# Performance work log

Measured on AMD Instinct MI355X. Metric: run time of the kernel, lower is better.

## Reference

```python
import jax, jax.numpy as jnp
from jax import lax
import numpy as np

VOCAB, TAGS, EMB, HID = 50000, 45, 256, 512
B, S = 32, 256


def setup_inputs() -> dict:
    key = jax.random.key(0)
    ks = jax.random.split(key, 12)
    sc = 0.05
    return {
        "x": jax.random.randint(ks[0], (B, S), 0, VOCAB),
        "tags": jax.random.randint(ks[1], (B, S), 0, TAGS),
        "emb": jax.random.normal(ks[2], (VOCAB, EMB), jnp.float32) * sc,
        "w_ih_f": jax.random.normal(ks[3], (4 * HID, EMB), jnp.float32) * sc,
        "w_hh_f": jax.random.normal(ks[4], (4 * HID, HID), jnp.float32) * sc,
        "b_f": jnp.zeros((4 * HID,), jnp.float32),
        "w_ih_b": jax.random.normal(ks[5], (4 * HID, EMB), jnp.float32) * sc,
        "w_hh_b": jax.random.normal(ks[6], (4 * HID, HID), jnp.float32) * sc,
        "b_b": jnp.zeros((4 * HID,), jnp.float32),
        "lin_w": jax.random.normal(ks[7], (TAGS, 2 * HID), jnp.float32) * sc,
        "lin_b": jnp.zeros((TAGS,), jnp.float32),
        "start_t": jax.random.normal(ks[8], (TAGS,), jnp.float32) * 0.1,
        "end_t": jax.random.normal(ks[9], (TAGS,), jnp.float32) * 0.1,
        "trans": jax.random.normal(ks[10], (TAGS,), jnp.float32)[:, None] * 0.0 + jax.random.normal(ks[11], (TAGS, TAGS), jnp.float32) * 0.1,
    }


def _lstm_dir(xs, w_ih, w_hh, b, reverse):
    # xs: [B,S,E]. PyTorch gate order: i, f, g, o.
    Bsz = xs.shape[0]
    H = w_hh.shape[1]
    def step(carry, x_t):
        h, c = carry
        g = x_t @ w_ih.T + h @ w_hh.T + b
        i, f, gg, o = jnp.split(g, 4, axis=-1)
        c = jax.nn.sigmoid(f) * c + jax.nn.sigmoid(i) * jnp.tanh(gg)
        h = jax.nn.sigmoid(o) * jnp.tanh(c)
        return (h, c), h
    init = (jnp.zeros((Bsz, H), xs.dtype), jnp.zeros((Bsz, H), xs.dtype))
    _, hs = lax.scan(step, init, jnp.swapaxes(xs, 0, 1), reverse=reverse)
    return jnp.swapaxes(hs, 0, 1)  # [B,S,H]


def _crf_nll(em, tags, start_t, end_t, trans):
    # em: [B,S,T]; numerator: score of gold path
    em_sc = jnp.take_along_axis(em, tags[..., None], axis=2)[..., 0].sum(axis=1)
    tr_sc = trans[tags[:, :-1], tags[:, 1:]].sum(axis=1)
    score = start_t[tags[:, 0]] + em_sc + tr_sc + end_t[tags[:, -1]]
    # partition function via forward algorithm (logsumexp recurrence)
    alpha0 = start_t + em[:, 0]  # [B,T]
    def step(alpha, e_t):
        alpha = jax.nn.logsumexp(alpha[:, :, None] + trans[None], axis=1) + e_t
        return alpha, None
    alpha, _ = lax.scan(step, alpha0, jnp.swapaxes(em[:, 1:], 0, 1))
    logZ = jax.nn.logsumexp(alpha + end_t, axis=1)
    return -(score - logZ).mean()  # reduction='mean', loss = -llh


def reference(x, tags, emb, w_ih_f, w_hh_f, b_f, w_ih_b, w_hh_b, b_b,
              lin_w, lin_b, start_t, end_t, trans):
    embeds = emb[x]                               # [B,S,E]
    h_f = _lstm_dir(embeds, w_ih_f, w_hh_f, b_f, False)
    h_b = _lstm_dir(embeds, w_ih_b, w_hh_b, b_b, True)
    lstm_out = jnp.concatenate([h_f, h_b], axis=-1)  # [B,S,2H]
    emissions = lstm_out @ lin_w.T + lin_b           # [B,S,T]
    return _crf_nll(emissions, tags, start_t, end_t, trans)
```

## Files before the change

### kernel.cpp

```cpp
#include <hip/hip_runtime.h>

#define BB 32
#define SS 256
#define EMBD 256
#define HIDD 512
#define NTAG 45
#define TPAD 48
#define NBLK 32
#define ROWS 64
#define APAD 520
#define GRID_REC 256

typedef __bf16 bf16x8 __attribute__((ext_vector_type(8)));
typedef float  f32x4  __attribute__((ext_vector_type(4)));
typedef short  s16x8  __attribute__((ext_vector_type(8)));

__device__ __forceinline__ unsigned short f2bf(float x) {
  unsigned u = __builtin_bit_cast(unsigned, x);
  u = (u + 0x7fffu + ((u >> 16) & 1u)) >> 16;
  return (unsigned short)u;
}
__device__ __forceinline__ float bf2f(unsigned short u) {
  unsigned v = ((unsigned)u) << 16; return __builtin_bit_cast(float, v);
}

__device__ __forceinline__ unsigned ld32_cpol(const unsigned* p, bool sys) {
  unsigned v;
  if (sys) asm volatile("global_load_dword %0, %1, off sc0 sc1\ns_waitcnt vmcnt(0)"
                        : "=v"(v) : "v"(p) : "memory");
  else     asm volatile("global_load_dword %0, %1, off sc0\ns_waitcnt vmcnt(0)"
                        : "=v"(v) : "v"(p) : "memory");
  return v;
}
__device__ __forceinline__ void st32_cpol(unsigned* p, unsigned v, bool sys) {
  if (sys) asm volatile("global_store_dword %0, %1, off sc0 sc1" :: "v"(p), "v"(v) : "memory");
  else     asm volatile("global_store_dword %0, %1, off sc0"     :: "v"(p), "v"(v) : "memory");
}

#define LD8(CPOL)                                                           \
  asm volatile("global_load_dwordx4 %0, %[q0], off " CPOL "\n\t"            \
               "global_load_dwordx4 %1, %[q1], off " CPOL "\n\t"            \
               "global_load_dwordx4 %2, %[q2], off " CPOL "\n\t"            \
               "global_load_dwordx4 %3, %[q3], off " CPOL "\n\t"            \
               "global_load_dwordx4 %4, %[q4], off " CPOL "\n\t"            \
               "global_load_dwordx4 %5, %[q5], off " CPOL "\n\t"            \
               "global_load_dwordx4 %6, %[q6], off " CPOL "\n\t"            \
               "global_load_dwordx4 %7, %[q7], off " CPOL "\n\t"            \
               "s_waitcnt vmcnt(0)"                                         \
               : "=&v"(v0), "=&v"(v1), "=&v"(v2), "=&v"(v3),                \
                 "=&v"(v4), "=&v"(v5), "=&v"(v6), "=&v"(v7)                 \
               : [q0] "v"(p), [q1] "v"(p + 2048), [q2] "v"(p + 4096),       \
                 [q3] "v"(p + 6144), [q4] "v"(p + 8192), [q5] "v"(p + 10240),\
                 [q6] "v"(p + 12288), [q7] "v"(p + 14336)                   \
               : "memory")

__global__ void k_pack_e(const int* __restrict__ x, const float* __restrict__ emb,
                         unsigned short* __restrict__ E) {
  int idx = blockIdx.x * 256 + threadIdx.x;
  int e = idx & 255; int bt = idx >> 8; int b = bt & 31; int t = bt >> 5;
  int tok = x[b * SS + t];
  E[idx] = f2bf(emb[(long)tok * EMBD + e]);
}

__global__ void k_pack_w(const float* __restrict__ wih_f, const float* __restrict__ whh_f,
                         const float* __restrict__ bf_,  const float* __restrict__ wih_b,
                         const float* __restrict__ whh_b, const float* __restrict__ bb_,
                         unsigned short* __restrict__ Wh, unsigned short* __restrict__ Wie,
                         float* __restrict__ Bh) {
  long idx = (long)blockIdx.x * 256 + threadIdx.x;
  int k = (int)(idx % 768); long rest = idx / 768;
  int r2 = (int)(rest & 2047); int dir = (int)(rest >> 11);
  int blk = r2 >> 6, rl = r2 & 63, gate = rl >> 4, hl = rl & 15;
  int orig = gate * HIDD + blk * 16 + hl;
  const float* wih = dir ? wih_b : wih_f;
  const float* whh = dir ? whh_b : whh_f;
  if (k < HIDD) Wh[((long)(dir * 2048 + r2)) * 512 + k] = f2bf(whh[(long)orig * HIDD + k]);
  else          Wie[((long)(dir * 2048 + r2)) * 256 + (k - 512)] = f2bf(wih[(long)orig * EMBD + (k - 512)]);
  if (k == 0) {
    const float* bias = dir ? bb_ : bf_;
    Bh[dir * 2048 + r2] = bias[orig];
  }
}

__global__ void k_pack_l(const float* __restrict__ lin_w, const float* __restrict__ lin_b,
                         unsigned short* __restrict__ LW, float* __restrict__ LB) {
  int idx = blockIdx.x * 256 + threadIdx.x;
  if (idx < TPAD * 1024) {
    int tag = idx >> 10; int c = idx & 1023;
    LW[idx] = (tag < NTAG) ? f2bf(lin_w[tag * 1024 + c]) : (unsigned short)0;
  } else if (idx < TPAD * 1024 + TPAD) {
    int tag = idx - TPAD * 1024;
    LB[tag] = (tag < NTAG) ? lin_b[tag] : 0.f;
  }
}

__launch_bounds__(256)
__global__ void k_eproj(const unsigned short* __restrict__ E,
                        const unsigned short* __restrict__ Wie,
                        const float* __restrict__ Bh,
                        unsigned short* __restrict__ Ep) {
  __shared__ unsigned short W2[64 * 264];
  const int bx = blockIdx.x;
  const int tg = bx & 63, blk = (bx >> 6) & 31, dir = bx >> 11;
  const int tid = threadIdx.x;
  const int w = tid >> 6, lane = tid & 63;
  const int lm = lane & 15, quad = lane >> 4;

  {
    const unsigned short* src = Wie + ((long)(dir * 2048 + blk * 64)) * 256;
    for (int i = 0; i < 8; ++i) {
      int c = i * 256 + tid;
      int row = c >> 5, off = c & 31;
      *(s16x8*)&W2[row * 264 + off * 8] = *(const s16x8*)&src[row * 256 + off * 8];
    }
  }
  __syncthreads();

  f32x4 acc[2][4] = {};
#pragma unroll
  for (int kk = 0; kk < 8; ++kk) {
    s16x8 av[2];
#pragma unroll
    for (int sub = 0; sub < 2; ++sub)
      av[sub] = *(const s16x8*)&E[((long)(tg * 128 + w * 32 + sub * 16 + lm)) * 256 + kk * 32 + quad * 8];
#pragma unroll
    for (int sub = 0; sub < 2; ++sub)
#pragma unroll
      for (int n = 0; n < 4; ++n) {
        s16x8 bs = *(const s16x8*)&W2[(n * 16 + lm) * 264 + kk * 32 + quad * 8];
        acc[sub][n] = __builtin_amdgcn_mfma_f32_16x16x32_bf16(
            __builtin_bit_cast(bf16x8, av[sub]), __builtin_bit_cast(bf16x8, bs), acc[sub][n], 0, 0, 0);
      }
  }
  float bh[4];
#pragma unroll
  for (int n = 0; n < 4; ++n) bh[n] = Bh[dir * 2048 + blk * 64 + n * 16 + lm];
#pragma unroll
  for (int sub = 0; sub < 2; ++sub)
#pragma unroll
    for (int n = 0; n < 4; ++n)
#pragma unroll
      for (int r = 0; r < 4; ++r) {
        int m = w * 32 + sub * 16 + quad * 4 + r;
        int t = tg * 4 + (m >> 5), b = m & 31;
        int row_l = n * 16 + lm;
        Ep[((((long)(dir * 32 + blk) * 256 + t) * 32 + b) * 64) + row_l] =
            f2bf(acc[sub][n][r] + bh[n]);
      }
}

__launch_bounds__(256, 1)
__global__ void k_rec(const unsigned short* __restrict__ Wh,
                      const unsigned short* __restrict__ Ep,
                      unsigned short* __restrict__ H,
                      unsigned int* __restrict__ sync) {
  __shared__ unsigned short A_ls[32 * APAD];
  __shared__ float G_ls[32 * 66 + 4608];
  __shared__ int fast_ls;

  const int bx = blockIdx.x;
  const int role = bx & 7;
  if (role >= 2) return;
  const int dir = role;
  const int blk = bx >> 3;
  const int tid = threadIdx.x;
  const int w = tid >> 6, lane = tid & 63;
  const int lm = lane & 15, quad = lane >> 4;
  const int mt = w >> 1, nt = w & 1;

  unsigned int* det   = sync;
  unsigned int* flags = sync + 64;

  s16x8 wb[2][16];
  {
    const unsigned short* wsrc =
        Wh + ((long)(dir * 2048 + blk * 64 + nt * 32 + lm)) * 512 + quad * 8;
#pragma unroll
    for (int ns = 0; ns < 2; ++ns)
#pragma unroll
      for (int kk = 0; kk < 16; ++kk)
        wb[ns][kk] = *(const s16x8*)&wsrc[ns * 16 * 512 + kk * 32];
  }

  unsigned xcc;
  asm volatile("s_getreg_b32 %0, hwreg(HW_REG_XCC_ID)" : "=s"(xcc));
  if (tid == 0) st32_cpol(&det[dir * 32 + blk], xcc | 0x100u, true);
  if (w == 0) {
    unsigned v;
    for (;;) {
      v = (lane < 32) ? ld32_cpol(&det[dir * 32 + lane], true) : (xcc | 0x100u);
      if (__ballot(v != 0u) == ~0ull) break;
      __builtin_amdgcn_s_sleep(1);
    }
    if (lane == 0) fast_ls = (__ballot(v == (xcc | 0x100u)) == ~0ull) ? 1 : 0;
  }
  __syncthreads();
  const bool fast = (fast_ls != 0);
  __threadfence();

  const int gb = tid >> 3, hp = tid & 7;
  float c0 = 0.f, c1 = 0.f;

  unsigned short* Hd = H + (long)dir * SS * BB * HIDD;
  unsigned int* flagd = flags + dir * SS * NBLK;
  const unsigned short* Epd = Ep + ((long)(dir * 32 + blk) * 256) * 32 * 64;

  for (int t = 0; t < SS; ++t) {
    const int tE = (dir == 0) ? t : (SS - 1 - t);

    unsigned short epv[8];
    {
      const unsigned short* eb =
          Epd + ((long)tE * 32 + (mt * 16 + quad * 4)) * 64 + nt * 32 + lm;
#pragma unroll
      for (int ns = 0; ns < 2; ++ns)
#pragma unroll
        for (int r = 0; r < 4; ++r) epv[ns * 4 + r] = eb[r * 64 + ns * 16];
    }

    f32x4 acc0 = {0.f, 0.f, 0.f, 0.f}, acc1 = {0.f, 0.f, 0.f, 0.f};
    if (t > 0) {
      if (w == 0) {
        const unsigned int* fl = flagd + (long)(t - 1) * NBLK;
        for (;;) {
          unsigned f = (lane < 32) ? ld32_cpol(&fl[lane], !fast) : 1u;
          if (__ballot(f != 0u) == ~0ull) break;
          __builtin_amdgcn_s_sleep(1);
        }
      }
      __syncthreads();
      {
        const int hslot = (dir == 0) ? (t - 1) : (SS - t);
        const unsigned short* p = Hd + (long)hslot * BB * HIDD + w * 512 + lane * 8;
        s16x8 v0, v1, v2, v3, v4, v5, v6, v7;
        if (fast) { LD8("sc0"); } else { LD8("sc0 sc1"); }
        unsigned short* d = &A_ls[w * APAD + lane * 8];
        *(s16x8*)(d + 0 * 2080) = v0; *(s16x8*)(d + 1 * 2080) = v1;
        *(s16x8*)(d + 2 * 2080) = v2; *(s16x8*)(d + 3 * 2080) = v3;
        *(s16x8*)(d + 4 * 2080) = v4; *(s16x8*)(d + 5 * 2080) = v5;
        *(s16x8*)(d + 6 * 2080) = v6; *(s16x8*)(d + 7 * 2080) = v7;
      }
      __syncthreads();
#pragma unroll
      for (int kk = 0; kk < 16; ++kk) {
        s16x8 av = *(const s16x8*)&A_ls[(mt * 16 + lm) * APAD + kk * 32 + quad * 8];
        acc0 = __builtin_amdgcn_mfma_f32_16x16x32_bf16(
            __builtin_bit_cast(bf16x8, av), __builtin_bit_cast(bf16x8, wb[0][kk]), acc0, 0, 0, 0);
        acc1 = __builtin_amdgcn_mfma_f32_16x16x32_bf16(
            __builtin_bit_cast(bf16x8, av), __builtin_bit_cast(bf16x8, wb[1][kk]), acc1, 0, 0, 0);
      }
    }
#pragma unroll
    for (int r = 0; r < 4; ++r) {
      int mm = mt * 16 + quad * 4 + r;
      G_ls[mm * 66 + nt * 32 + lm]      = acc0[r] + bf2f(epv[r]);
      G_ls[mm * 66 + nt * 32 + 16 + lm] = acc1[r] + bf2f(epv[4 + r]);
    }
    __syncthreads();
    {
      float gi0 = G_ls[gb * 66 + 0  + 2 * hp], gi1 = G_ls[gb * 66 + 0  + 2 * hp + 1];
      float gf0 = G_ls[gb * 66 + 16 + 2 * hp], gf1 = G_ls[gb * 66 + 16 + 2 * hp + 1];
      float gg0 = G_ls[gb * 66 + 32 + 2 * hp], gg1 = G_ls[gb * 66 + 32 + 2 * hp + 1];
      float go0 = G_ls[gb * 66 + 48 + 2 * hp], go1 = G_ls[gb * 66 + 48 + 2 * hp + 1];
      float si0 = 1.f / (1.f + __expf(-gi0)), si1 = 1.f / (1.f + __expf(-gi1));
      float sf0 = 1.f / (1.f + __expf(-gf0)), sf1 = 1.f / (1.f + __expf(-gf1));
      float so0 = 1.f / (1.f + __expf(-go0)), so1 = 1.f / (1.f + __expf(-go1));
      float tg0 = tanhf(gg0), tg1 = tanhf(gg1);
      c0 = sf0 * c0 + si0 * tg0;
      c1 = sf1 * c1 + si1 * tg1;
      float h0 = so0 * tanhf(c0), h1 = so1 * tanhf(c1);
      int tslot = (dir == 0) ? t : (SS - 1 - t);
      unsigned hv = (unsigned)f2bf(h0) | ((unsigned)f2bf(h1) << 16);
      st32_cpol((unsigned*)&Hd[(long)tslot * BB * HIDD + (long)gb * HIDD + blk * 16 + 2 * hp],
                hv, !fast);
    }
    __syncthreads();
    if (t < SS - 1 && tid == 0)
      st32_cpol(&flagd[(long)t * NBLK + blk], 1u, !fast);
  }
}

__launch_bounds__(256)
__global__ void k_emis(const unsigned short* __restrict__ H,
                       const unsigned short* __restrict__ LW,
                       const float* __restrict__ LB,
                       float* __restrict__ EM) {
  const int row0 = blockIdx.x * 32;
  const int tid = threadIdx.x;
  const int w = tid >> 6, lane = tid & 63;
  const int lm = lane & 15, quad = lane >> 4;
  const unsigned short* Hf = H;
  const unsigned short* Hb = H + (long)SS * BB * HIDD;

  for (int tile = w; tile < 6; tile += 4) {
    int mt = tile / 3, nt = tile % 3;
    int arow = row0 + mt * 16 + lm;
    int nrow = nt * 16 + lm;
    f32x4 acc = {0.f, 0.f, 0.f, 0.f};
#pragma unroll 4
    for (int kk = 0; kk < 32; ++kk) {
      int k0 = kk * 32 + quad * 8;
      s16x8 asv = (k0 < HIDD) ? *(const s16x8*)&Hf[(long)arow * HIDD + k0]
                              : *(const s16x8*)&Hb[(long)arow * HIDD + (k0 - HIDD)];
      s16x8 bsv = *(const s16x8*)&LW[nrow * 1024 + k0];
      acc = __builtin_amdgcn_mfma_f32_16x16x32_bf16(
          __builtin_bit_cast(bf16x8, asv), __builtin_bit_cast(bf16x8, bsv), acc, 0, 0, 0);
    }
    float bias = LB[nrow];
#pragma unroll
    for (int r = 0; r < 4; ++r) {
      int mm = row0 + mt * 16 + quad * 4 + r;
      EM[(long)mm * TPAD + nrow] = acc[r] + bias;
    }
  }
}

__global__ void k_crf(const int* __restrict__ tags, const float* __restrict__ start_t,
                      const float* __restrict__ end_t, const float* __restrict__ trans,
                      const float* __restrict__ EM, float* __restrict__ chain) {
  __shared__ float T_ls[NTAG * TPAD];
  __shared__ float ET[48 * 48 + 16];
  __shared__ float P_ls[64];
  const int b = blockIdx.x;
  const int lane = threadIdx.x;
  const int j = lane;

  for (int i = lane; i < NTAG * NTAG; i += 64)
    T_ls[(i / NTAG) * TPAD + (i % NTAG)] = trans[i];
  for (int i = lane; i < 48 * 48 + 16; i += 64) ET[i] = 0.f;
  __syncthreads();

  float Mj = -1e30f;
  if (j < NTAG) {
    for (int i = 0; i < NTAG; ++i) Mj = fmaxf(Mj, T_ls[i * TPAD + j]);
    for (int i = 0; i < NTAG; ++i) ET[i * 48 + j] = __expf(T_ls[i * TPAD + j] - Mj);
  }
  __syncthreads();

  float et[48];
#pragma unroll
  for (int i = 0; i < 48; ++i) et[i] = ET[i * 48 + j];

  float part = 0.f;
  for (int t = lane; t < SS; t += 64) {
    int tg = tags[b * SS + t];
    part += EM[((long)t * BB + b) * TPAD + tg];
    if (t + 1 < SS) part += T_ls[tg * TPAD + tags[b * SS + t + 1]];
    if (t == 0)      part += start_t[tg];
    if (t == SS - 1) part += end_t[tg];
  }
  for (int off = 32; off; off >>= 1) part += __shfl_down(part, off);
  float score = __shfl(part, 0);

  float alpha = (j < NTAG) ? (start_t[j] + EM[(long)b * TPAD + j]) : -1e30f;
  float e_next = (j < NTAG) ? EM[((long)BB + b) * TPAD + j] : 0.f;
  for (int t = 1; t < SS; ++t) {
    float e_cur = e_next;
    if (t < SS - 1) e_next = (j < NTAG) ? EM[((long)(t + 1) * BB + b) * TPAD + j] : 0.f;
    float am = alpha;
#pragma unroll
    for (int off = 32; off; off >>= 1) am = fmaxf(am, __shfl_xor(am, off));
    float p = __expf(alpha - am);
    P_ls[lane] = p;
    __builtin_amdgcn_wave_barrier();
    float s0 = 0.f, s1 = 0.f, s2 = 0.f, s3 = 0.f;
#pragma unroll
    for (int i0 = 0; i0 < 48; i0 += 4) {
      f32x4 pv = *(const f32x4*)&P_ls[i0];
      s0 += pv.x * et[i0];
      s1 += pv.y * et[i0 + 1];
      s2 += pv.z * et[i0 + 2];
      s3 += pv.w * et[i0 + 3];
    }
    __builtin_amdgcn_wave_barrier();
    float s = (s0 + s1) + (s2 + s3);
    float na = am + Mj + __logf(s) + e_cur;
    alpha = (j < NTAG) ? na : -1e30f;
  }
  float v = (j < NTAG) ? (alpha + end_t[j]) : -1e30f;
  float mx = v;
  for (int off = 32; off; off >>= 1) mx = fmaxf(mx, __shfl_xor(mx, off));
  float s = __expf(v - mx);
  for (int off = 32; off; off >>= 1) s += __shfl_xor(s, off);
  if (lane == 0) chain[b] = score - (mx + __logf(s));
}

__global__ void k_fin(const float* __restrict__ chain, float* __restrict__ out) {
  int lane = threadIdx.x;
  float v = (lane < BB) ? chain[lane] : 0.f;
  for (int off = 32; off; off >>= 1) v += __shfl_xor(v, off);
  if (lane == 0) out[0] = -v / (float)BB;
}

extern "C" void kernel_launch(void* const* d_in, const int* in_sizes, int n_in,
                              void* d_out, int out_size, void* d_ws, size_t ws_size,
                              hipStream_t stream) {
  const int*   x      = (const int*)d_in[0];
  const int*   tags   = (const int*)d_in[1];
  const float* emb    = (const float*)d_in[2];
  const float* wih_f  = (const float*)d_in[3];
  const float* whh_f  = (const float*)d_in[4];
  const float* b_f    = (const float*)d_in[5];
  const float* wih_b  = (const float*)d_in[6];
  const float* whh_b  = (const float*)d_in[7];
  const float* b_b    = (const float*)d_in[8];
  const float* lin_w  = (const float*)d_in[9];
  const float* lin_b  = (const float*)d_in[10];
  const float* start_t= (const float*)d_in[11];
  const float* end_t  = (const float*)d_in[12];
  const float* trans  = (const float*)d_in[13];

  char* ws = (char*)d_ws;
  size_t off = 0;
  auto alloc = [&](size_t bytes) {
    void* p = ws + off; off = (off + bytes + 255) & ~(size_t)255; return p;
  };
  size_t sync_bytes = (64 + 2 * SS * NBLK) * 4;
  unsigned int*   sync = (unsigned int*) alloc(sync_bytes);
  unsigned short* E   = (unsigned short*)alloc((size_t)SS * BB * EMBD * 2);
  unsigned short* Wh  = (unsigned short*)alloc((size_t)2 * 2048 * 512 * 2);
  unsigned short* Wie = (unsigned short*)alloc((size_t)2 * 2048 * 256 * 2);
  float*          Bh  = (float*)         alloc((size_t)2 * 2048 * 4);
  unsigned short* Ep  = (unsigned short*)alloc((size_t)2 * 32 * 256 * 32 * 64 * 2);
  unsigned short* H   = (unsigned short*)alloc((size_t)2 * SS * BB * HIDD * 2);
  unsigned short* LW  = (unsigned short*)alloc((size_t)TPAD * 1024 * 2);
  float*          LB  = (float*)         alloc((size_t)TPAD * 4);
  float*          EM  = (float*)         alloc((size_t)SS * BB * TPAD * 4);
  float*          chain = (float*)       alloc((size_t)BB * 4);

  hipMemsetAsync(sync, 0, sync_bytes, stream);
  k_pack_e<<<dim3((SS * BB * EMBD) / 256), dim3(256), 0, stream>>>(x, emb, E);
  k_pack_w<<<dim3((2 * 2048 * 768) / 256), dim3(256), 0, stream>>>(
      wih_f, whh_f, b_f, wih_b, whh_b, b_b, Wh, Wie, Bh);
  k_pack_l<<<dim3((TPAD * 1024 + TPAD + 255) / 256), dim3(256), 0, stream>>>(
      lin_w, lin_b, LW, LB);
  k_eproj<<<dim3(4096), dim3(256), 0, stream>>>(E, Wie, Bh, Ep);

  void* kargs[] = {&Wh, &Ep, &H, &sync};
  hipLaunchCooperativeKernel((const void*)k_rec, dim3(GRID_REC), dim3(256), kargs, 0, stream);

  k_emis<<<dim3((SS * BB) / 32), dim3(256), 0, stream>>>(H, LW, LB, EM);
  k_crf<<<dim3(BB), dim3(64), 0, stream>>>(tags, start_t, end_t, trans, EM, chain);
  k_fin<<<dim3(1), dim3(64), 0, stream>>>(chain, (float*)d_out);
}
```

Measured before the change: 1.081 ms.

## Halve recurrence blocks to 16 per direction with 512-thread blocks and per-wave flags

Restructures the persistent LSTM recurrence kernel so each direction uses 16 blocks of 512 threads. Each block now owns 32 hidden units instead of 16, which halves the number of blocks that must synchronise each timestep. The input-projection output is repacked so each thread loads its gate preactivations with a single vector load, and that load is prefetched one step ahead. The block-wide barrier before the flag store is replaced by per-wave flags after a vmcnt wait, and tanhf is replaced by an exp-based approximation. In exchange, each block carries more per-step work, there are more flag words to poll, and the fast tanh may lose some accuracy.

```diff
diff --git a/kernel.cpp b/kernel.cpp
--- a/kernel.cpp
+++ b/kernel.cpp
@@ -6,14 +6,15 @@
 #define HIDD 512
 #define NTAG 45
 #define TPAD 48
-#define NBLK 32
-#define ROWS 64
+#define NBLK 16
 #define APAD 520
-#define GRID_REC 256
+#define PADG 132
+#define GRID_REC 128
 
 typedef __bf16 bf16x8 __attribute__((ext_vector_type(8)));
 typedef float  f32x4  __attribute__((ext_vector_type(4)));
 typedef short  s16x8  __attribute__((ext_vector_type(8)));
+typedef short  s16x4  __attribute__((ext_vector_type(4)));
 
 __device__ __forceinline__ unsigned short f2bf(float x) {
   unsigned u = __builtin_bit_cast(unsigned, x);
@@ -22,6 +23,10 @@
 }
 __device__ __forceinline__ float bf2f(unsigned short u) {
   unsigned v = ((unsigned)u) << 16; return __builtin_bit_cast(float, v);
+}
+__device__ __forceinline__ float ftanh(float x) {
+  float e = __expf(2.f * x);
+  return 1.f - 2.f / (e + 1.f);
 }
 
 __device__ __forceinline__ unsigned ld32_cpol(const unsigned* p, bool sys) {
@@ -36,22 +41,28 @@
   if (sys) asm volatile("global_store_dword %0, %1, off sc0 sc1" :: "v"(p), "v"(v) : "memory");
   else     asm volatile("global_store_dword %0, %1, off sc0"     :: "v"(p), "v"(v) : "memory");
 }
-
-#define LD8(CPOL)                                                           \
+__device__ __forceinline__ unsigned ld32x2_cpol(const unsigned* p0, const unsigned* p1, bool sys) {
+  unsigned a, b;
+  if (sys) asm volatile("global_load_dword %0, %2, off sc0 sc1\n\t"
+                        "global_load_dword %1, %3, off sc0 sc1\n\t"
+                        "s_waitcnt vmcnt(0)"
+                        : "=&v"(a), "=&v"(b) : "v"(p0), "v"(p1) : "memory");
+  else     asm volatile("global_load_dword %0, %2, off sc0\n\t"
+                        "global_load_dword %1, %3, off sc0\n\t"
+                        "s_waitcnt vmcnt(0)"
+                        : "=&v"(a), "=&v"(b) : "v"(p0), "v"(p1) : "memory");
+  return a & b;
+}
+
+#define LD4(CPOL)                                                           \
   asm volatile("global_load_dwordx4 %0, %[q0], off " CPOL "\n\t"            \
                "global_load_dwordx4 %1, %[q1], off " CPOL "\n\t"            \
                "global_load_dwordx4 %2, %[q2], off " CPOL "\n\t"            \
                "global_load_dwordx4 %3, %[q3], off " CPOL "\n\t"            \
-               "global_load_dwordx4 %4, %[q4], off " CPOL "\n\t"            \
-               "global_load_dwordx4 %5, %[q5], off " CPOL "\n\t"            \
-               "global_load_dwordx4 %6, %[q6], off " CPOL "\n\t"            \
-               "global_load_dwordx4 %7, %[q7], off " CPOL "\n\t"            \
                "s_waitcnt vmcnt(0)"                                         \
-               : "=&v"(v0), "=&v"(v1), "=&v"(v2), "=&v"(v3),                \
-                 "=&v"(v4), "=&v"(v5), "=&v"(v6), "=&v"(v7)                 \
-               : [q0] "v"(p), [q1] "v"(p + 2048), [q2] "v"(p + 4096),       \
-                 [q3] "v"(p + 6144), [q4] "v"(p + 8192), [q5] "v"(p + 10240),\
-                 [q6] "v"(p + 12288), [q7] "v"(p + 14336)                   \
+               : "=&v"(v0), "=&v"(v1), "=&v"(v2), "=&v"(v3)                 \
+               : [q0] "v"(p), [q1] "v"(p + 4096), [q2] "v"(p + 8192),       \
+                 [q3] "v"(p + 12288)                                        \
                : "memory")
 
 __global__ void k_pack_e(const int* __restrict__ x, const float* __restrict__ emb,
@@ -70,15 +81,22 @@
   long idx = (long)blockIdx.x * 256 + threadIdx.x;
   int k = (int)(idx % 768); long rest = idx / 768;
   int r2 = (int)(rest & 2047); int dir = (int)(rest >> 11);
-  int blk = r2 >> 6, rl = r2 & 63, gate = rl >> 4, hl = rl & 15;
-  int orig = gate * HIDD + blk * 16 + hl;
   const float* wih = dir ? wih_b : wih_f;
   const float* whh = dir ? whh_b : whh_f;
-  if (k < HIDD) Wh[((long)(dir * 2048 + r2)) * 512 + k] = f2bf(whh[(long)orig * HIDD + k]);
-  else          Wie[((long)(dir * 2048 + r2)) * 256 + (k - 512)] = f2bf(wih[(long)orig * EMBD + (k - 512)]);
+  if (k < HIDD) {
+    int blkN = r2 >> 7, gateN = (r2 >> 5) & 3, hlN = r2 & 31;
+    int origN = gateN * HIDD + blkN * 32 + hlN;
+    Wh[((long)(dir * 2048 + r2)) * 512 + k] = f2bf(whh[(long)origN * HIDD + k]);
+  } else {
+    int blkO = r2 >> 6, gateO = (r2 >> 4) & 3, hlO = r2 & 15;
+    int origO = gateO * HIDD + blkO * 16 + hlO;
+    Wie[((long)(dir * 2048 + r2)) * 256 + (k - 512)] = f2bf(wih[(long)origO * EMBD + (k - 512)]);
+  }
   if (k == 0) {
+    int blkO = r2 >> 6, gateO = (r2 >> 4) & 3, hlO = r2 & 15;
+    int origO = gateO * HIDD + blkO * 16 + hlO;
     const float* bias = dir ? bb_ : bf_;
-    Bh[dir * 2048 + r2] = bias[orig];
+    Bh[dir * 2048 + r2] = bias[origO];
   }
 }
 
@@ -135,27 +153,28 @@
   float bh[4];
 #pragma unroll
   for (int n = 0; n < 4; ++n) bh[n] = Bh[dir * 2048 + blk * 64 + n * 16 + lm];
+
+  const int t = tg * 4 + w;
+  const int b16 = blk >> 1, nsb = blk & 1;
 #pragma unroll
   for (int sub = 0; sub < 2; ++sub)
 #pragma unroll
-    for (int n = 0; n < 4; ++n)
-#pragma unroll
-      for (int r = 0; r < 4; ++r) {
-        int m = w * 32 + sub * 16 + quad * 4 + r;
-        int t = tg * 4 + (m >> 5), b = m & 31;
-        int row_l = n * 16 + lm;
-        Ep[((((long)(dir * 32 + blk) * 256 + t) * 32 + b) * 64) + row_l] =
-            f2bf(acc[sub][n][r] + bh[n]);
-      }
-}
-
-__launch_bounds__(256, 1)
+    for (int n = 0; n < 4; ++n) {
+      int tidp = (sub * 4 + n) * 64 + quad * 16 + lm;
+      s16x4 pk;
+#pragma unroll
+      for (int r = 0; r < 4; ++r) pk[r] = (short)f2bf(acc[sub][n][r] + bh[n]);
+      *(s16x4*)&Ep[((((long)(dir * NBLK + b16) * SS + t) * 512) + tidp) * 8 + nsb * 4] = pk;
+    }
+}
+
+__launch_bounds__(512, 2)
 __global__ void k_rec(const unsigned short* __restrict__ Wh,
                       const unsigned short* __restrict__ Ep,
                       unsigned short* __restrict__ H,
                       unsigned int* __restrict__ sync) {
   __shared__ unsigned short A_ls[32 * APAD];
-  __shared__ float G_ls[32 * 66 + 4608];
+  __shared__ float G_ls[32 * PADG];
   __shared__ int fast_ls;
 
   const int bx = blockIdx.x;
@@ -166,7 +185,7 @@
   const int tid = threadIdx.x;
   const int w = tid >> 6, lane = tid & 63;
   const int lm = lane & 15, quad = lane >> 4;
-  const int mt = w >> 1, nt = w & 1;
+  const int msub = w >> 2, ntg = w & 3;
 
   unsigned int* det   = sync;
   unsigned int* flags = sync + 64;
@@ -174,7 +193,7 @@
   s16x8 wb[2][16];
   {
     const unsigned short* wsrc =
-        Wh + ((long)(dir * 2048 + blk * 64 + nt * 32 + lm)) * 512 + quad * 8;
+        Wh + ((long)(dir * 2048 + blk * 128 + ntg * 32 + lm)) * 512 + quad * 8;
 #pragma unroll
     for (int ns = 0; ns < 2; ++ns)
 #pragma unroll
@@ -188,7 +207,7 @@
   if (w == 0) {
     unsigned v;
     for (;;) {
-      v = (lane < 32) ? ld32_cpol(&det[dir * 32 + lane], true) : (xcc | 0x100u);
+      v = (lane < NBLK) ? ld32_cpol(&det[dir * 32 + lane], true) : (xcc | 0x100u);
       if (__ballot(v != 0u) == ~0ull) break;
       __builtin_amdgcn_s_sleep(1);
     }
@@ -198,32 +217,23 @@
   const bool fast = (fast_ls != 0);
   __threadfence();
 
-  const int gb = tid >> 3, hp = tid & 7;
+  const int gb = tid >> 4, hp = tid & 15;
   float c0 = 0.f, c1 = 0.f;
 
   unsigned short* Hd = H + (long)dir * SS * BB * HIDD;
-  unsigned int* flagd = flags + dir * SS * NBLK;
-  const unsigned short* Epd = Ep + ((long)(dir * 32 + blk) * 256) * 32 * 64;
+  unsigned int* flagd = flags + dir * SS * NBLK * 8;
+  const unsigned short* Epd = Ep + ((long)(dir * NBLK + blk)) * SS * 4096;
+
+  s16x8 ecur = *(const s16x8*)&Epd[(long)(dir ? (SS - 1) : 0) * 4096 + tid * 8];
+  s16x8 enext;
 
   for (int t = 0; t < SS; ++t) {
-    const int tE = (dir == 0) ? t : (SS - 1 - t);
-
-    unsigned short epv[8];
-    {
-      const unsigned short* eb =
-          Epd + ((long)tE * 32 + (mt * 16 + quad * 4)) * 64 + nt * 32 + lm;
-#pragma unroll
-      for (int ns = 0; ns < 2; ++ns)
-#pragma unroll
-        for (int r = 0; r < 4; ++r) epv[ns * 4 + r] = eb[r * 64 + ns * 16];
-    }
-
     f32x4 acc0 = {0.f, 0.f, 0.f, 0.f}, acc1 = {0.f, 0.f, 0.f, 0.f};
     if (t > 0) {
       if (w == 0) {
-        const unsigned int* fl = flagd + (long)(t - 1) * NBLK;
+        const unsigned int* fl = flagd + (long)(t - 1) * (NBLK * 8);
         for (;;) {
-          unsigned f = (lane < 32) ? ld32_cpol(&fl[lane], !fast) : 1u;
+          unsigned f = ld32x2_cpol(&fl[lane], &fl[lane + 64], !fast);
           if (__ballot(f != 0u) == ~0ull) break;
           __builtin_amdgcn_s_sleep(1);
         }
@@ -231,52 +241,62 @@
       __syncthreads();
       {
         const int hslot = (dir == 0) ? (t - 1) : (SS - t);
-        const unsigned short* p = Hd + (long)hslot * BB * HIDD + w * 512 + lane * 8;
-        s16x8 v0, v1, v2, v3, v4, v5, v6, v7;
-        if (fast) { LD8("sc0"); } else { LD8("sc0 sc1"); }
+        const unsigned short* p = Hd + (long)hslot * (BB * HIDD) + w * 512 + lane * 8;
+        s16x8 v0, v1, v2, v3;
+        if (fast) { LD4("sc0"); } else { LD4("sc0 sc1"); }
         unsigned short* d = &A_ls[w * APAD + lane * 8];
-        *(s16x8*)(d + 0 * 2080) = v0; *(s16x8*)(d + 1 * 2080) = v1;
-        *(s16x8*)(d + 2 * 2080) = v2; *(s16x8*)(d + 3 * 2080) = v3;
-        *(s16x8*)(d + 4 * 2080) = v4; *(s16x8*)(d + 5 * 2080) = v5;
-        *(s16x8*)(d + 6 * 2080) = v6; *(s16x8*)(d + 7 * 2080) = v7;
+        *(s16x8*)(d + 0 * 8 * APAD) = v0;
+        *(s16x8*)(d + 1 * 8 * APAD) = v1;
+        *(s16x8*)(d + 2 * 8 * APAD) = v2;
+        *(s16x8*)(d + 3 * 8 * APAD) = v3;
       }
       __syncthreads();
+      {
+        int tn = (t < SS - 1) ? t + 1 : t;
+        int tEn = (dir == 0) ? tn : (SS - 1 - tn);
+        enext = *(const s16x8*)&Epd[(long)tEn * 4096 + tid * 8];
+      }
 #pragma unroll
       for (int kk = 0; kk < 16; ++kk) {
-        s16x8 av = *(const s16x8*)&A_ls[(mt * 16 + lm) * APAD + kk * 32 + quad * 8];
+        s16x8 av = *(const s16x8*)&A_ls[(msub * 16 + lm) * APAD + kk * 32 + quad * 8];
         acc0 = __builtin_amdgcn_mfma_f32_16x16x32_bf16(
             __builtin_bit_cast(bf16x8, av), __builtin_bit_cast(bf16x8, wb[0][kk]), acc0, 0, 0, 0);
         acc1 = __builtin_amdgcn_mfma_f32_16x16x32_bf16(
             __builtin_bit_cast(bf16x8, av), __builtin_bit_cast(bf16x8, wb[1][kk]), acc1, 0, 0, 0);
       }
+    } else {
+      int tEn = (dir == 0) ? 1 : (SS - 2);
+      enext = *(const s16x8*)&Epd[(long)tEn * 4096 + tid * 8];
     }
 #pragma unroll
     for (int r = 0; r < 4; ++r) {
-      int mm = mt * 16 + quad * 4 + r;
-      G_ls[mm * 66 + nt * 32 + lm]      = acc0[r] + bf2f(epv[r]);
-      G_ls[mm * 66 + nt * 32 + 16 + lm] = acc1[r] + bf2f(epv[4 + r]);
+      int m = msub * 16 + quad * 4 + r;
+      G_ls[m * PADG + ntg * 32 + lm]      = acc0[r] + bf2f((unsigned short)ecur[r]);
+      G_ls[m * PADG + ntg * 32 + 16 + lm] = acc1[r] + bf2f((unsigned short)ecur[4 + r]);
     }
     __syncthreads();
     {
-      float gi0 = G_ls[gb * 66 + 0  + 2 * hp], gi1 = G_ls[gb * 66 + 0  + 2 * hp + 1];
-      float gf0 = G_ls[gb * 66 + 16 + 2 * hp], gf1 = G_ls[gb * 66 + 16 + 2 * hp + 1];
-      float gg0 = G_ls[gb * 66 + 32 + 2 * hp], gg1 = G_ls[gb * 66 + 32 + 2 * hp + 1];
-      float go0 = G_ls[gb * 66 + 48 + 2 * hp], go1 = G_ls[gb * 66 + 48 + 2 * hp + 1];
-      float si0 = 1.f / (1.f + __expf(-gi0)), si1 = 1.f / (1.f + __expf(-gi1));
-      float sf0 = 1.f / (1.f + __expf(-gf0)), sf1 = 1.f / (1.f + __expf(-gf1));
-      float so0 = 1.f / (1.f + __expf(-go0)), so1 = 1.f / (1.f + __expf(-go1));
-      float tg0 = tanhf(gg0), tg1 = tanhf(gg1);
+      const float* g0 = &G_ls[gb * PADG + 2 * hp];
+      float2 gi = *(const float2*)(g0 + 0);
+      float2 gf = *(const float2*)(g0 + 32);
+      float2 gg = *(const float2*)(g0 + 64);
+      float2 go = *(const float2*)(g0 + 96);
+      float si0 = 1.f / (1.f + __expf(-gi.x)), si1 = 1.f / (1.f + __expf(-gi.y));
+      float sf0 = 1.f / (1.f + __expf(-gf.x)), sf1 = 1.f / (1.f + __expf(-gf.y));
+      float so0 = 1.f / (1.f + __expf(-go.x)), so1 = 1.f / (1.f + __expf(-go.y));
+      float tg0 = ftanh(gg.x), tg1 = ftanh(gg.y);
       c0 = sf0 * c0 + si0 * tg0;
       c1 = sf1 * c1 + si1 * tg1;
-      float h0 = so0 * tanhf(c0), h1 = so1 * tanhf(c1);
+      float h0 = so0 * ftanh(c0), h1 = so1 * ftanh(c1);
       int tslot = (dir == 0) ? t : (SS - 1 - t);
       unsigned hv = (unsigned)f2bf(h0) | ((unsigned)f2bf(h1) << 16);
-      st32_cpol((unsigned*)&Hd[(long)tslot * BB * HIDD + (long)gb * HIDD + blk * 16 + 2 * hp],
+      st32_cpol((unsigned*)&Hd[(long)tslot * (BB * HIDD) + (long)gb * HIDD + blk * 32 + 2 * hp],
                 hv, !fast);
     }
-    __syncthreads();
-    if (t < SS - 1 && tid == 0)
-      st32_cpol(&flagd[(long)t * NBLK + blk], 1u, !fast);
+    asm volatile("s_waitcnt vmcnt(0)" ::: "memory");
+    if (t < SS - 1 && lane == 0)
+      st32_cpol(&flagd[(long)t * (NBLK * 8) + blk * 8 + w], 1u, !fast);
+    ecur = enext;
   }
 }
 
@@ -415,13 +435,13 @@
   auto alloc = [&](size_t bytes) {
     void* p = ws + off; off = (off + bytes + 255) & ~(size_t)255; return p;
   };
-  size_t sync_bytes = (64 + 2 * SS * NBLK) * 4;
+  size_t sync_bytes = (64 + 2 * SS * NBLK * 8) * 4;
   unsigned int*   sync = (unsigned int*) alloc(sync_bytes);
   unsigned short* E   = (unsigned short*)alloc((size_t)SS * BB * EMBD * 2);
   unsigned short* Wh  = (unsigned short*)alloc((size_t)2 * 2048 * 512 * 2);
   unsigned short* Wie = (unsigned short*)alloc((size_t)2 * 2048 * 256 * 2);
   float*          Bh  = (float*)         alloc((size_t)2 * 2048 * 4);
-  unsigned short* Ep  = (unsigned short*)alloc((size_t)2 * 32 * 256 * 32 * 64 * 2);
+  unsigned short* Ep  = (unsigned short*)alloc((size_t)2 * NBLK * SS * 512 * 8 * 2);
   unsigned short* H   = (unsigned short*)alloc((size_t)2 * SS * BB * HIDD * 2);
   unsigned short* LW  = (unsigned short*)alloc((size_t)TPAD * 1024 * 2);
   float*          LB  = (float*)         alloc((size_t)TPAD * 4);
@@ -437,7 +457,7 @@
   k_eproj<<<dim3(4096), dim3(256), 0, stream>>>(E, Wie, Bh, Ep);
 
   void* kargs[] = {&Wh, &Ep, &H, &sync};
-  hipLaunchCooperativeKernel((const void*)k_rec, dim3(GRID_REC), dim3(256), kargs, 0, stream);
+  hipLaunchCooperativeKernel((const void*)k_rec, dim3(GRID_REC), dim3(512), kargs, 0, stream);
 
   k_emis<<<dim3((SS * BB) / 32), dim3(256), 0, stream>>>(H, LW, LB, EM);
   k_crf<<<dim3(BB), dim3(64), 0, stream>>>(tags, start_t, end_t, trans, EM, chain);
```

Result: slower. 1.257 ms (+16.2%).

## Per-wave flags, prefetched input-projection tiles, and fast tanh in LSTM recurrence

Applied to the files above, without the earlier changes.

Changes the precomputed input-projection layout so each thread reads its eight gate values with one 16-byte vector load, and prefetches the next timestep's values during the current step. It replaces the end-of-step block barrier with per-wave completion flags (four per block), so waiters poll 128 flags with paired loads. It also swaps tanhf for an exp-based tanh. These target per-step latency on the serial recurrence, at the cost of more flag traffic and slightly different tanh accuracy.

```diff
diff --git a/kernel.cpp b/kernel.cpp
--- a/kernel.cpp
+++ b/kernel.cpp
@@ -14,6 +14,7 @@
 typedef __bf16 bf16x8 __attribute__((ext_vector_type(8)));
 typedef float  f32x4  __attribute__((ext_vector_type(4)));
 typedef short  s16x8  __attribute__((ext_vector_type(8)));
+typedef short  s16x4  __attribute__((ext_vector_type(4)));
 
 __device__ __forceinline__ unsigned short f2bf(float x) {
   unsigned u = __builtin_bit_cast(unsigned, x);
@@ -22,6 +23,10 @@
 }
 __device__ __forceinline__ float bf2f(unsigned short u) {
   unsigned v = ((unsigned)u) << 16; return __builtin_bit_cast(float, v);
+}
+__device__ __forceinline__ float ftanh(float x) {
+  float e = __expf(2.f * x);
+  return 1.f - 2.f / (e + 1.f);
 }
 
 __device__ __forceinline__ unsigned ld32_cpol(const unsigned* p, bool sys) {
@@ -35,6 +40,18 @@
 __device__ __forceinline__ void st32_cpol(unsigned* p, unsigned v, bool sys) {
   if (sys) asm volatile("global_store_dword %0, %1, off sc0 sc1" :: "v"(p), "v"(v) : "memory");
   else     asm volatile("global_store_dword %0, %1, off sc0"     :: "v"(p), "v"(v) : "memory");
+}
+__device__ __forceinline__ unsigned ld32x2_cpol(const unsigned* p0, const unsigned* p1, bool sys) {
+  unsigned a, b;
+  if (sys) asm volatile("global_load_dword %0, %2, off sc0 sc1\n\t"
+                        "global_load_dword %1, %3, off sc0 sc1\n\t"
+                        "s_waitcnt vmcnt(0)"
+                        : "=&v"(a), "=&v"(b) : "v"(p0), "v"(p1) : "memory");
+  else     asm volatile("global_load_dword %0, %2, off sc0\n\t"
+                        "global_load_dword %1, %3, off sc0\n\t"
+                        "s_waitcnt vmcnt(0)"
+                        : "=&v"(a), "=&v"(b) : "v"(p0), "v"(p1) : "memory");
+  return a & b;
 }
 
 #define LD8(CPOL)                                                           \
@@ -135,18 +152,18 @@
   float bh[4];
 #pragma unroll
   for (int n = 0; n < 4; ++n) bh[n] = Bh[dir * 2048 + blk * 64 + n * 16 + lm];
+
+  const int t = tg * 4 + w;
 #pragma unroll
   for (int sub = 0; sub < 2; ++sub)
 #pragma unroll
-    for (int n = 0; n < 4; ++n)
-#pragma unroll
-      for (int r = 0; r < 4; ++r) {
-        int m = w * 32 + sub * 16 + quad * 4 + r;
-        int t = tg * 4 + (m >> 5), b = m & 31;
-        int row_l = n * 16 + lm;
-        Ep[((((long)(dir * 32 + blk) * 256 + t) * 32 + b) * 64) + row_l] =
-            f2bf(acc[sub][n][r] + bh[n]);
-      }
+    for (int n = 0; n < 4; ++n) {
+      s16x4 pk;
+#pragma unroll
+      for (int r = 0; r < 4; ++r) pk[r] = (short)f2bf(acc[sub][n][r] + bh[n]);
+      int tidc = (sub * 2 + (n >> 1)) * 64 + quad * 16 + lm;
+      *(s16x4*)&Ep[(((long)(dir * 32 + blk) * SS + t) * 256 + tidc) * 8 + (n & 1) * 4] = pk;
+    }
 }
 
 __launch_bounds__(256, 1)
@@ -202,28 +219,19 @@
   float c0 = 0.f, c1 = 0.f;
 
   unsigned short* Hd = H + (long)dir * SS * BB * HIDD;
-  unsigned int* flagd = flags + dir * SS * NBLK;
-  const unsigned short* Epd = Ep + ((long)(dir * 32 + blk) * 256) * 32 * 64;
+  unsigned int* flagd = flags + dir * SS * NBLK * 4;
+  const unsigned short* Epd = Ep + (long)(dir * 32 + blk) * SS * 2048;
+
+  s16x8 ecur = *(const s16x8*)&Epd[((long)(dir ? (SS - 1) : 0) * 256 + tid) * 8];
+  s16x8 enext;
 
   for (int t = 0; t < SS; ++t) {
-    const int tE = (dir == 0) ? t : (SS - 1 - t);
-
-    unsigned short epv[8];
-    {
-      const unsigned short* eb =
-          Epd + ((long)tE * 32 + (mt * 16 + quad * 4)) * 64 + nt * 32 + lm;
-#pragma unroll
-      for (int ns = 0; ns < 2; ++ns)
-#pragma unroll
-        for (int r = 0; r < 4; ++r) epv[ns * 4 + r] = eb[r * 64 + ns * 16];
-    }
-
     f32x4 acc0 = {0.f, 0.f, 0.f, 0.f}, acc1 = {0.f, 0.f, 0.f, 0.f};
     if (t > 0) {
       if (w == 0) {
-        const unsigned int* fl = flagd + (long)(t - 1) * NBLK;
+        const unsigned int* fl = flagd + (long)(t - 1) * (NBLK * 4);
         for (;;) {
-          unsigned f = (lane < 32) ? ld32_cpol(&fl[lane], !fast) : 1u;
+          unsigned f = ld32x2_cpol(&fl[lane], &fl[lane + 64], !fast);
           if (__ballot(f != 0u) == ~0ull) break;
           __builtin_amdgcn_s_sleep(1);
         }
@@ -241,6 +249,11 @@
         *(s16x8*)(d + 6 * 2080) = v6; *(s16x8*)(d + 7 * 2080) = v7;
       }
       __syncthreads();
+      {
+        int tn = (t < SS - 1) ? t + 1 : t;
+        int tEn = (dir == 0) ? tn : (SS - 1 - tn);
+        enext = *(const s16x8*)&Epd[((long)tEn * 256 + tid) * 8];
+      }
 #pragma unroll
       for (int kk = 0; kk < 16; ++kk) {
         s16x8 av = *(const s16x8*)&A_ls[(mt * 16 + lm) * APAD + kk * 32 + quad * 8];
@@ -249,12 +262,15 @@
         acc1 = __builtin_amdgcn_mfma_f32_16x16x32_bf16(
             __builtin_bit_cast(bf16x8, av), __builtin_bit_cast(bf16x8, wb[1][kk]), acc1, 0, 0, 0);
       }
+    } else {
+      int tEn = (dir == 0) ? 1 : (SS - 2);
+      enext = *(const s16x8*)&Epd[((long)tEn * 256 + tid) * 8];
     }
 #pragma unroll
     for (int r = 0; r < 4; ++r) {
       int mm = mt * 16 + quad * 4 + r;
-      G_ls[mm * 66 + nt * 32 + lm]      = acc0[r] + bf2f(epv[r]);
-      G_ls[mm * 66 + nt * 32 + 16 + lm] = acc1[r] + bf2f(epv[4 + r]);
+      G_ls[mm * 66 + nt * 32 + lm]      = acc0[r] + bf2f((unsigned short)ecur[r]);
+      G_ls[mm * 66 + nt * 32 + 16 + lm] = acc1[r] + bf2f((unsigned short)ecur[4 + r]);
     }
     __syncthreads();
     {
@@ -265,18 +281,19 @@
       float si0 = 1.f / (1.f + __expf(-gi0)), si1 = 1.f / (1.f + __expf(-gi1));
       float sf0 = 1.f / (1.f + __expf(-gf0)), sf1 = 1.f / (1.f + __expf(-gf1));
       float so0 = 1.f / (1.f + __expf(-go0)), so1 = 1.f / (1.f + __expf(-go1));
-      float tg0 = tanhf(gg0), tg1 = tanhf(gg1);
+      float tg0 = ftanh(gg0), tg1 = ftanh(gg1);
       c0 = sf0 * c0 + si0 * tg0;
       c1 = sf1 * c1 + si1 * tg1;
-      float h0 = so0 * tanhf(c0), h1 = so1 * tanhf(c1);
+      float h0 = so0 * ftanh(c0), h1 = so1 * ftanh(c1);
       int tslot = (dir == 0) ? t : (SS - 1 - t);
       unsigned hv = (unsigned)f2bf(h0) | ((unsigned)f2bf(h1) << 16);
       st32_cpol((unsigned*)&Hd[(long)tslot * BB * HIDD + (long)gb * HIDD + blk * 16 + 2 * hp],
                 hv, !fast);
     }
-    __syncthreads();
-    if (t < SS - 1 && tid == 0)
-      st32_cpol(&flagd[(long)t * NBLK + blk], 1u, !fast);
+    asm volatile("s_waitcnt vmcnt(0)" ::: "memory");
+    if (t < SS - 1 && lane == 0)
+      st32_cpol(&flagd[(long)t * (NBLK * 4) + blk * 4 + w], 1u, !fast);
+    ecur = enext;
   }
 }
 
@@ -415,13 +432,13 @@
   auto alloc = [&](size_t bytes) {
     void* p = ws + off; off = (off + bytes + 255) & ~(size_t)255; return p;
   };
-  size_t sync_bytes = (64 + 2 * SS * NBLK) * 4;
+  size_t sync_bytes = (64 + 2 * SS * NBLK * 4) * 4;
   unsigned int*   sync = (unsigned int*) alloc(sync_bytes);
   unsigned short* E   = (unsigned short*)alloc((size_t)SS * BB * EMBD * 2);
   unsigned short* Wh  = (unsigned short*)alloc((size_t)2 * 2048 * 512 * 2);
   unsigned short* Wie = (unsigned short*)alloc((size_t)2 * 2048 * 256 * 2);
   float*          Bh  = (float*)         alloc((size_t)2 * 2048 * 4);
-  unsigned short* Ep  = (unsigned short*)alloc((size_t)2 * 32 * 256 * 32 * 64 * 2);
+  unsigned short* Ep  = (unsigned short*)alloc((size_t)2 * 32 * SS * 2048 * 2);
   unsigned short* H   = (unsigned short*)alloc((size_t)2 * SS * BB * HIDD * 2);
   unsigned short* LW  = (unsigned short*)alloc((size_t)TPAD * 1024 * 2);
   float*          LB  = (float*)         alloc((size_t)TPAD * 4);
```

Result: slower. 1.175 ms (+8.6%).
